# Optimization experiments

Hardware: AMD Instinct MI355X
Metric: run time of the kernel (lower is better)

## Reference

```python
import jax, jax.numpy as jnp
import numpy as np

B, T, M, F, H, O = 64, 168, 256, 32, 128, 32
TWO_OVER_PI = 2.0 / np.pi


def setup_inputs() -> dict:
    key = jax.random.key(0)
    ks = jax.random.split(key, 8)
    return {
        "x": jax.random.normal(ks[0], (B, T, M, F), dtype=jnp.float32),
        "assoc_W": jax.random.normal(ks[1], (F, M, M), dtype=jnp.float32) * (1.0 / np.sqrt(M)),
        "W_ih": jax.random.normal(ks[2], (4 * H, F), dtype=jnp.float32) * (1.0 / np.sqrt(F)),
        "W_hh": jax.random.normal(ks[3], (4 * H, H), dtype=jnp.float32) * (1.0 / np.sqrt(H)),
        "b_ih": jax.random.normal(ks[4], (4 * H,), dtype=jnp.float32) * 0.01,
        "b_hh": jax.random.normal(ks[5], (4 * H,), dtype=jnp.float32) * 0.01,
        "dense_W": jax.random.normal(ks[6], (O, H), dtype=jnp.float32) * (1.0 / np.sqrt(H)),
        "dense_b": jax.random.normal(ks[7], (O,), dtype=jnp.float32) * 0.01,
    }


def _forward(x, assoc_W, W_ih, W_hh, b_ih, b_hh, dense_W, dense_b):
    # x: [B, T, M, F] (batch_first) -> scan over time
    xt = jnp.transpose(x, (1, 0, 2, 3))  # [T, B, M, F]
    b, m = x.shape[0], x.shape[2]
    h0 = jnp.zeros((b, m, H), dtype=x.dtype)
    c0 = jnp.zeros((b, m, H), dtype=x.dtype)

    def step(carry, xin):
        h, c = carry
        # ArcTanNorm: squash into (-1, 1)
        y = jnp.arctan(xin) * TWO_OVER_PI                      # [B, M, F]
        # ICFA: per-attribute association across map units
        y = jnp.einsum('amn,bna->bma', assoc_W, y)             # [B, M, F]
        # LSTM cell (shared weights across map units), PyTorch gate order i,f,g,o
        gates = (jnp.einsum('bmf,gf->bmg', y, W_ih) + b_ih
                 + jnp.einsum('bmh,gh->bmg', h, W_hh) + b_hh)  # [B, M, 4H]
        i, f, g, o = jnp.split(gates, 4, axis=-1)
        i, f, o = jax.nn.sigmoid(i), jax.nn.sigmoid(f), jax.nn.sigmoid(o)
        g = jnp.tanh(g)
        c = f * c + i * g
        h = o * jnp.tanh(c)
        # Dense output head
        out = jnp.einsum('bmh,oh->bmo', h, dense_W) + dense_b  # [B, M, O]
        return (h, c), out

    _, outs = jax.lax.scan(step, (h0, c0), xt)                 # [T, B, M, O]
    return jnp.transpose(outs, (1, 0, 2, 3))                   # [B, T, M, O]


def reference(x, assoc_W, W_ih, W_hh, b_ih, b_hh, dense_W, dense_b):
    return _forward(x, assoc_W, W_ih, W_hh, b_ih, b_hh, dense_W, dense_b)
```

## Files before the change

kernel.cpp:

```cpp
#include <hip/hip_runtime.h>

#define B_  64
#define T_  168
#define M_  256
#define F_  32
#define H_  128
#define O_  32
#define BT_ (B_*T_)

typedef __attribute__((ext_vector_type(8))) short bh8;
typedef __attribute__((ext_vector_type(4))) short sh4;
typedef __attribute__((ext_vector_type(4))) float fx4;

static __device__ __forceinline__ short f2bf(float f) {
  unsigned u = __float_as_uint(f);
  u += 0x7FFFu + ((u >> 16) & 1u);
  return (short)(u >> 16);
}
static __device__ __forceinline__ unsigned cvtpk(float lo, float hi) {
  unsigned r;
  asm("v_cvt_pk_bf16_f32 %0, %1, %2" : "=v"(r) : "v"(lo), "v"(hi));
  return r;
}
static __device__ __forceinline__ float ex2_(float x) {
#if __has_builtin(__builtin_amdgcn_exp2f)
  return __builtin_amdgcn_exp2f(x);
#else
  return exp2f(x);
#endif
}
static __device__ __forceinline__ float rcp_(float x) {
#if __has_builtin(__builtin_amdgcn_rcpf)
  return __builtin_amdgcn_rcpf(x);
#else
  return 1.0f / x;
#endif
}
static __device__ __forceinline__ float sigm(float x) {
  return 1.0f / (1.0f + __expf(-x));
}
static __device__ __forceinline__ float tanh_f(float x) {
  return 1.0f - 2.0f / (1.0f + __expf(2.0f * x));
}
static __device__ __forceinline__ fx4 mm16(bh8 a, bh8 b, fx4 c) {
  return __builtin_amdgcn_mfma_f32_16x16x32_bf16(a, b, c, 0, 0, 0);
}
static __device__ __forceinline__ bh8 cvt8(fx4 p0, fx4 p1) {
  bh8 s;
  s[0] = f2bf(p0[0]); s[1] = f2bf(p0[1]); s[2] = f2bf(p0[2]); s[3] = f2bf(p0[3]);
  s[4] = f2bf(p1[0]); s[5] = f2bf(p1[1]); s[6] = f2bf(p1[2]); s[7] = f2bf(p1[3]);
  return s;
}


__global__ __launch_bounds__(512) void atan_tr(const float* __restrict__ x,
                                               short* __restrict__ ut) {
  __shared__ __align__(16) short tl[8 * 32 * 68];
  const int tid = threadIdx.x;
  const float c2p = 0.63661977236758134f;
  for (int it = 0; it < 21; ++it) {
    const int id = blockIdx.x + it * 256;
    const int bt0 = (id >> 2) * 8, n0 = (id & 3) * 64;
    if (it) __syncthreads();
#pragma unroll
    for (int i = 0; i < 8; ++i) {
      int idx = tid + i * 512;
      int aq = idx & 7, nl = (idx >> 3) & 63, btl = idx >> 9;
      const float* src = x + (long)(bt0 + btl) * 8192 + (n0 + nl) * 32 + aq * 4;
      fx4 v = *(const fx4*)src;
      int base = (btl * 32 + aq * 4) * 68 + nl;
#pragma unroll
      for (int k = 0; k < 4; ++k)
        tl[base + k * 68] = f2bf(atanf(v[k]) * c2p);
    }
    __syncthreads();
#pragma unroll
    for (int p = 0; p < 8; ++p) {
      int r = p * 32 + (tid >> 4);
      int a = r >> 3, btl = r & 7, nq = tid & 15;
      sh4 v = *(const sh4*)&tl[(btl * 32 + a) * 68 + nq * 4];
      *(sh4*)&ut[((long)a * BT_ + bt0 + btl) * 256 + n0 + nq * 4] = v;
    }
  }
}

__global__ __launch_bounds__(512) void icfa_gemm(const short* __restrict__ ut,
                                                 const float* __restrict__ aw,
                                                 short* __restrict__ y) {
  __shared__ __align__(16) short waf[8 * 8 * 64 * 8];
  __shared__ __align__(16) short ubf[64 * 256];
  const int tid = threadIdx.x;
  const int lane = tid & 63, w = tid >> 6, l15 = lane & 15, l4 = lane >> 4;
  const int a = blockIdx.x >> 3, s = blockIdx.x & 7;
  const long ua = (long)a * BT_;

  for (int mh = 0; mh < 2; ++mh) {
    __syncthreads();
    for (int i = 0; i < 8; ++i) {
      int idx = tid + i * 512;
      int ln = idx & 63, ks = (idx >> 6) & 7, mt = idx >> 9;
      const float* src = aw + a * 65536 + (mh * 128 + mt * 16 + (ln & 15)) * 256
                         + ks * 32 + (ln >> 4) * 8;
      *(bh8*)&waf[idx * 8] = cvt8(*(const fx4*)src, *(const fx4*)(src + 4));
    }
    __syncthreads();
    bh8 Af[8];
#pragma unroll
    for (int ks = 0; ks < 8; ++ks)
      Af[ks] = *(const bh8*)&waf[((w * 8 + ks) * 64 + lane) * 8];

    for (int tile = 0; tile < 21; ++tile) {
      const int bt0 = s * 1344 + tile * 64;
      __syncthreads();
#pragma unroll
      for (int i = 0; i < 4; ++i) {
        int idx = tid + i * 512;
        int row = idx >> 5, slot = idx & 31;
        bh8 v = *(const bh8*)&ut[(ua + bt0 + row) * 256 + slot * 8];
        int sb = (row * 512 + slot * 16) ^ ((row & 7) << 4);
        *(bh8*)&((char*)ubf)[sb] = v;
      }
      __syncthreads();
#pragma unroll
      for (int ct = 0; ct < 4; ++ct) {
        fx4 acc = {0.f, 0.f, 0.f, 0.f};
        const int btr = ct * 16 + l15;
#pragma unroll
        for (int ks = 0; ks < 8; ++ks) {
          int byo = (btr * 512 + ks * 64 + l4 * 16) ^ ((btr & 7) << 4);
          bh8 Bf = *(const bh8*)&((char*)ubf)[byo];
          acc = mm16(Af[ks], Bf, acc);
        }
        sh4 o;
        o[0] = f2bf(acc[0]); o[1] = f2bf(acc[1]);
        o[2] = f2bf(acc[2]); o[3] = f2bf(acc[3]);
        *(sh4*)&y[(ua + bt0 + btr) * 256 + mh * 128 + w * 16 + l4 * 4] = o;
      }
    }
  }
}

__global__ __launch_bounds__(1024) void lstm_fused4(
    const short* __restrict__ y,
    const float* __restrict__ Wih, const float* __restrict__ Whh,
    const float* __restrict__ bih, const float* __restrict__ bhh,
    const float* __restrict__ dW,  const float* __restrict__ db,
    float* __restrict__ out) {
  __shared__ __align__(16) short whf[65536];
  __shared__ __align__(16) short hx[8192];
  __shared__ __align__(16) short ytr[2048];
  const int tid = threadIdx.x;
  const int lane = tid & 63, w = tid >> 6, l15 = lane & 15, l4 = lane >> 4;
  const int wg = w & 7, hw = w >> 3;
  const int bidx = blockIdx.x >> 2, m0 = (blockIdx.x & 3) * 64;
  const float L2E = 1.4426950408889634f;

  for (int i = 0; i < 8; ++i) {
    int idx = tid + i * 1024;
    int ln = idx & 63, ks = (idx >> 6) & 3, gate = (idx >> 8) & 3, wgp = idx >> 10;
    const float* src = Whh + ((gate * 8 + wgp) * 16 + (ln & 15)) * 128
                       + ks * 32 + (ln >> 4) * 8;
    *(bh8*)&whf[idx * 8] = cvt8(*(const fx4*)src, *(const fx4*)(src + 4));
  }
  for (int i = 0; i < 4; ++i) ((int*)hx)[tid + i * 1024] = 0;

  bh8 wfih[4]; float nb[4];
#pragma unroll
  for (int gate = 0; gate < 4; ++gate) {
    int g = (gate * 8 + wg) * 16 + l15;
    float b = bih[g] + bhh[g];
    nb[gate] = (gate == 2) ? (2.0f * L2E * b) : (-L2E * b);
    const float* src = Wih + g * 32 + l4 * 8;
    wfih[gate] = cvt8(*(const fx4*)src, *(const fx4*)(src + 4));
  }
  bh8 df[4];
  const int rt_d = 2 * hw + (wg & 1), oc = (wg >> 1) & 1;
  const int od = oc * 16 + l15;
  const float dbias = db[od];
#pragma unroll
  for (int ks = 0; ks < 4; ++ks) {
    const float* src = dW + od * 128 + ks * 32 + l4 * 8;
    df[ks] = cvt8(*(const fx4*)src, *(const fx4*)(src + 4));
  }

  float cst[2][4];
#pragma unroll
  for (int rr = 0; rr < 2; ++rr)
#pragma unroll
    for (int r = 0; r < 4; ++r) cst[rr][r] = 0.f;

  const char* hxc = (const char*)hx;
  const int rbase = (hw * 32 + l15) * 64 + ((l4 * 16) ^ ((l15 >> 2) << 4));
  const int wbase = (wg >> 1) * 4096 + (hw * 32 + l4 * 4) * 64
                  + ((2 * ((wg & 1) * 16 + l15)) ^ (l4 << 4));
  const int dbase = rbase + (wg & 1) * 1024;
  const int wfb = wg * 16384 + lane * 16;
  const int ar = tid >> 5, mq2 = tid & 31;
  const long yrow = (long)ar * BT_ + (long)bidx * T_;
  const long obB = (long)bidx * T_ * 8192
                 + (long)(m0 + rt_d * 16 + l4 * 4) * 32 + od;

  int ys = *(const int*)&y[(yrow + 0) * 256 + m0 + mq2 * 2];
  {
    int ml0 = mq2 * 2, ml1 = ml0 + 1;
    ytr[((ml0 >> 4) * 64 + ((ar >> 3) << 4) + (ml0 & 15)) * 8 + (ar & 7)] =
        (short)(ys & 0xffff);
    ytr[((ml1 >> 4) * 64 + ((ar >> 3) << 4) + (ml1 & 15)) * 8 + (ar & 7)] =
        (short)(((unsigned)ys) >> 16);
  }
  ys = *(const int*)&y[(yrow + 1) * 256 + m0 + mq2 * 2];
  __syncthreads();

  for (int t = 0; t < T_; ++t) {
    int ysn = 0;
    if (t + 2 < T_) ysn = *(const int*)&y[(yrow + t + 2) * 256 + m0 + mq2 * 2];
    fx4 acc[2][4];
    {
      bh8 ya0 = *(const bh8*)&ytr[((2 * hw) * 64 + lane) * 8];
      bh8 ya1 = *(const bh8*)&ytr[((2 * hw + 1) * 64 + lane) * 8];
      fx4 Z = {0.f, 0.f, 0.f, 0.f};
#pragma unroll
      for (int g = 0; g < 4; ++g) {
        acc[0][g] = mm16(ya0, wfih[g], Z);
        acc[1][g] = mm16(ya1, wfih[g], Z);
      }
    }
#pragma unroll
    for (int ks = 0; ks < 4; ++ks) {
      bh8 h0 = *(const bh8*)(hxc + rbase + ks * 4096);
      bh8 h1 = *(const bh8*)(hxc + rbase + 1024 + ks * 4096);
#pragma unroll
      for (int g = 0; g < 4; ++g) {
        bh8 Bf = *(const bh8*)((const char*)whf + wfb + (g * 4 + ks) * 1024);
        acc[0][g] = mm16(h0, Bf, acc[0][g]);
        acc[1][g] = mm16(h1, Bf, acc[1][g]);
      }
    }
    if (wg < 4 && t > 0) {
      fx4 A = {dbias, dbias, dbias, dbias};
#pragma unroll
      for (int ks = 0; ks < 4; ++ks) {
        bh8 hd = *(const bh8*)(hxc + dbase + ks * 4096);
        A = mm16(hd, df[ks], A);
      }
      float* op = out + obB + (long)(t - 1) * 8192;
#pragma unroll
      for (int ri = 0; ri < 4; ++ri) op[ri * 32] = A[ri];
    }
    float hn[2][4];
#pragma unroll
    for (int rr = 0; rr < 2; ++rr)
#pragma unroll
      for (int r = 0; r < 4; ++r) {
        float iv = rcp_(1.f + ex2_(fmaf(acc[rr][0][r], -L2E, nb[0])));
        float fv = rcp_(1.f + ex2_(fmaf(acc[rr][1][r], -L2E, nb[1])));
        float ov = rcp_(1.f + ex2_(fmaf(acc[rr][3][r], -L2E, nb[3])));
        float gv = 1.f - 2.f * rcp_(1.f + ex2_(fmaf(acc[rr][2][r], 2.f * L2E, nb[2])));
        float cn = fv * cst[rr][r] + iv * gv;
        cst[rr][r] = cn;
        float th = 1.f - 2.f * rcp_(1.f + ex2_(cn * (2.f * L2E)));
        hn[rr][r] = ov * th;
      }
    __syncthreads();
#pragma unroll
    for (int rr = 0; rr < 2; ++rr) {
      unsigned p01 = cvtpk(hn[rr][0], hn[rr][1]);
      unsigned p23 = cvtpk(hn[rr][2], hn[rr][3]);
      short* bp = (short*)((char*)hx + wbase + rr * 1024);
      bp[0]  = (short)(p01 & 0xffff);
      bp[32] = (short)(p01 >> 16);
      bp[64] = (short)(p23 & 0xffff);
      bp[96] = (short)(p23 >> 16);
    }
    if (t + 1 < T_) {
      int ml0 = mq2 * 2, ml1 = ml0 + 1;
      ytr[((ml0 >> 4) * 64 + ((ar >> 3) << 4) + (ml0 & 15)) * 8 + (ar & 7)] =
          (short)(ys & 0xffff);
      ytr[((ml1 >> 4) * 64 + ((ar >> 3) << 4) + (ml1 & 15)) * 8 + (ar & 7)] =
          (short)(((unsigned)ys) >> 16);
    }
    ys = ysn;
    __syncthreads();
  }
  if (wg < 4) {
    fx4 A = {dbias, dbias, dbias, dbias};
#pragma unroll
    for (int ks = 0; ks < 4; ++ks) {
      bh8 hd = *(const bh8*)(hxc + dbase + ks * 4096);
      A = mm16(hd, df[ks], A);
    }
    float* op = out + obB + (long)(T_ - 1) * 8192;
#pragma unroll
    for (int ri = 0; ri < 4; ++ri) op[ri * 32] = A[ri];
  }
}


__global__ __launch_bounds__(512) void icfa_mfma(const float* __restrict__ x,
                                                 const float* __restrict__ aw,
                                                 float* __restrict__ y) {
  __shared__ short waf[8 * 8 * 64 * 8];
  __shared__ short ubf[64 * 264];
  const int tid = threadIdx.x;
  const int lane = tid & 63, w = tid >> 6, l15 = lane & 15, l4 = lane >> 4;
  const int a = blockIdx.x >> 3, s = blockIdx.x & 7;
  const float c2p = 0.63661977236758134f;

  for (int mh = 0; mh < 2; ++mh) {
    __syncthreads();
    for (int i = 0; i < 8; ++i) {
      int idx = tid + i * 512;
      int ln = idx & 63, ks = (idx >> 6) & 7, mt = idx >> 9;
      const float* src = aw + a * 65536 + (mh * 128 + mt * 16 + (ln & 15)) * 256
                         + ks * 32 + (ln >> 4) * 8;
      *(bh8*)&waf[idx * 8] = cvt8(*(const fx4*)src, *(const fx4*)(src + 4));
    }
    __syncthreads();
    bh8 Af[8];
#pragma unroll
    for (int ks = 0; ks < 8; ++ks)
      Af[ks] = *(const bh8*)&waf[((w * 8 + ks) * 64 + lane) * 8];

    for (int tile = 0; tile < 21; ++tile) {
      const int bt0 = s * 1344 + tile * 64;
      __syncthreads();
#pragma unroll 4
      for (int i = 0; i < 32; ++i) {
        int idx = tid + i * 512;
        int n = idx & 255, btc = idx >> 8;
        float v = x[(long)(bt0 + btc) * 8192 + n * 32 + a];
        ubf[btc * 264 + n] = f2bf(atanf(v) * c2p);
      }
      __syncthreads();
#pragma unroll
      for (int ct = 0; ct < 4; ++ct) {
        fx4 acc = {0.f, 0.f, 0.f, 0.f};
#pragma unroll
        for (int ks = 0; ks < 8; ++ks) {
          bh8 Bf = *(const bh8*)&ubf[(ct * 16 + l15) * 264 + ks * 32 + l4 * 8];
          acc = mm16(Af[ks], Bf, acc);
        }
        long ybase = (long)(bt0 + ct * 16 + l15) * 8192
                     + (mh * 128 + w * 16 + l4 * 4) * 32 + a;
#pragma unroll
        for (int r = 0; r < 4; ++r) y[ybase + (long)r * 32] = acc[r];
      }
    }
  }
}

__global__ __launch_bounds__(512) void lstm_fused(
    const float* __restrict__ Wih, const float* __restrict__ Whh,
    const float* __restrict__ bih, const float* __restrict__ bhh,
    const float* __restrict__ dW,  const float* __restrict__ db,
    float* __restrict__ yo) {
  __shared__ short whf[32 * 4 * 64 * 8];
  __shared__ short hbuf[4 * 4 * 64 * 8];
  __shared__ short ytr[4 * 64 * 8];
  __shared__ float obuf[64 * 36];
  const int tid = threadIdx.x;
  const int lane = tid & 63, w = tid >> 6, l15 = lane & 15, l4 = lane >> 4;
  const int bidx = blockIdx.x >> 2, m0 = (blockIdx.x & 3) * 64;

  for (int i = 0; i < 16; ++i) {
    int idx = tid + i * 512;
    int ln = idx & 63, ks = (idx >> 6) & 3, ct = idx >> 8;
    const float* src = Whh + (ct * 16 + (ln & 15)) * 128 + ks * 32 + (ln >> 4) * 8;
    *(bh8*)&whf[idx * 8] = cvt8(*(const fx4*)src, *(const fx4*)(src + 4));
  }
  for (int i = 0; i < 8; ++i) ((int*)hbuf)[tid + i * 512] = 0;

  bh8 wfih[4]; float bias[4];
#pragma unroll
  for (int gate = 0; gate < 4; ++gate) {
    int g = (gate * 8 + w) * 16 + l15;
    bias[gate] = bih[g] + bhh[g];
    const float* src = Wih + g * 32 + l4 * 8;
    wfih[gate] = cvt8(*(const fx4*)src, *(const fx4*)(src + 4));
  }
  bh8 df[4];
  const int rtd = w >> 1, oc = w & 1;
  const int od = oc * 16 + l15;
  const float dbias = db[od];
#pragma unroll
  for (int ks = 0; ks < 4; ++ks) {
    const float* src = dW + od * 128 + ks * 32 + l4 * 8;
    df[ks] = cvt8(*(const fx4*)src, *(const fx4*)(src + 4));
  }

  float cst[4][4];
#pragma unroll
  for (int rt = 0; rt < 4; ++rt)
#pragma unroll
    for (int r = 0; r < 4; ++r) cst[rt][r] = 0.f;

  const int mloc = tid >> 3, a0 = (tid & 7) * 4;
  const long tb0 = (long)bidx * T_ * 8192;
  const long pfoff = (long)(m0 + mloc) * 32 + a0;
  const int ytre = ((mloc >> 4) * 64 + ((a0 >> 3) << 4) + (mloc & 15)) * 8 + (a0 & 7);
  const int kse = w >> 1;
  const int lnhi = (((w & 1) * 2 + (l15 >> 3)) << 4);
  const int e0 = l15 & 7;

  fx4 y4 = *(const fx4*)&yo[tb0 + pfoff];
  {
    sh4 p; p[0] = f2bf(y4[0]); p[1] = f2bf(y4[1]); p[2] = f2bf(y4[2]); p[3] = f2bf(y4[3]);
    *(sh4*)&ytr[ytre] = p;
  }
  y4 = *(const fx4*)&yo[tb0 + 8192 + pfoff];
  __syncthreads();

  for (int t = 0; t < T_; ++t) {
    const long off = tb0 + (long)t * 8192;
    float hn[4][4];
    bh8 Ball[4][4];
#pragma unroll
    for (int gate = 0; gate < 4; ++gate)
#pragma unroll
      for (int ks = 0; ks < 4; ++ks)
        Ball[gate][ks] =
            *(const bh8*)&whf[((((gate * 8 + w) * 4) + ks) * 64 + lane) * 8];
#pragma unroll
    for (int rt = 0; rt < 4; ++rt) {
      bh8 ya = *(const bh8*)&ytr[(rt * 64 + lane) * 8];
      bh8 hA[4];
#pragma unroll
      for (int ks = 0; ks < 4; ++ks)
        hA[ks] = *(const bh8*)&hbuf[((rt * 4 + ks) * 64 + lane) * 8];
      fx4 acc[4];
#pragma unroll
      for (int gate = 0; gate < 4; ++gate) {
        fx4 A = {bias[gate], bias[gate], bias[gate], bias[gate]};
        A = mm16(ya, wfih[gate], A);
#pragma unroll
        for (int ks = 0; ks < 4; ++ks) A = mm16(hA[ks], Ball[gate][ks], A);
        acc[gate] = A;
      }
#pragma unroll
      for (int r = 0; r < 4; ++r) {
        float iv = sigm(acc[0][r]);
        float fv = sigm(acc[1][r]);
        float gv = tanh_f(acc[2][r]);
        float ov = sigm(acc[3][r]);
        float cn = fv * cst[rt][r] + iv * gv;
        cst[rt][r] = cn;
        hn[rt][r] = ov * tanh_f(cn);
      }
    }
    __syncthreads();
#pragma unroll
    for (int rt = 0; rt < 4; ++rt)
#pragma unroll
      for (int r = 0; r < 4; ++r)
        hbuf[((rt * 4 + kse) * 64 + lnhi + l4 * 4 + r) * 8 + e0] = f2bf(hn[rt][r]);
    if (t + 1 < T_) {
      sh4 p; p[0] = f2bf(y4[0]); p[1] = f2bf(y4[1]); p[2] = f2bf(y4[2]); p[3] = f2bf(y4[3]);
      *(sh4*)&ytr[ytre] = p;
    }
    if (t + 2 < T_) y4 = *(const fx4*)&yo[off + 2 * 8192 + pfoff];
    __syncthreads();
    {
      fx4 A = {dbias, dbias, dbias, dbias};
#pragma unroll
      for (int ks = 0; ks < 4; ++ks) {
        bh8 hA2 = *(const bh8*)&hbuf[((rtd * 4 + ks) * 64 + lane) * 8];
        A = mm16(hA2, df[ks], A);
      }
#pragma unroll
      for (int r = 0; r < 4; ++r)
        obuf[(rtd * 16 + l4 * 4 + r) * 36 + oc * 16 + l15] = A[r];
    }
    __syncthreads();
    {
      fx4 o4 = *(const fx4*)&obuf[mloc * 36 + a0];
      *(fx4*)&yo[off + pfoff] = o4;
    }
  }
}

extern "C" void kernel_launch(void* const* d_in, const int* in_sizes, int n_in,
                              void* d_out, int out_size, void* d_ws, size_t ws_size,
                              hipStream_t stream) {
  const float* x   = (const float*)d_in[0];
  const float* aw  = (const float*)d_in[1];
  const float* wih = (const float*)d_in[2];
  const float* whh = (const float*)d_in[3];
  const float* bih = (const float*)d_in[4];
  const float* bhh = (const float*)d_in[5];
  const float* dw  = (const float*)d_in[6];
  const float* db  = (const float*)d_in[7];
  float* out = (float*)d_out;

  const size_t PLANE = (size_t)32 * BT_ * 256;
  const size_t NEED  = 2 * PLANE * sizeof(short);
  if (d_ws && ws_size >= NEED) {
    short* u = (short*)d_ws;
    short* yv = u + PLANE;
    hipLaunchKernelGGL(atan_tr,   dim3(256), dim3(512), 0, stream, x, u);
    hipLaunchKernelGGL(icfa_gemm, dim3(256), dim3(512), 0, stream, u, aw, yv);
    hipLaunchKernelGGL(lstm_fused4, dim3(256), dim3(1024), 0, stream,
                       yv, wih, whh, bih, bhh, dw, db, out);
  } else {
    hipLaunchKernelGGL(icfa_mfma, dim3(256), dim3(512), 0, stream, x, aw, out);
    hipLaunchKernelGGL(lstm_fused, dim3(256), dim3(512), 0, stream,
                       wih, whh, bih, bhh, dw, db, out);
  }
}
```

Before: 856.2 us.

## Transpose LSTM MFMA operands so h-state stores and output writes vectorize

The LSTM recurrence kernel swaps the A/B operands of its MFMAs, so gates come out along the hidden dimension with rows per lane. The h buffer moves to a padded row-major layout (272-byte stride), which turns the four scattered 2-byte stores per tile into one 8-byte store. The dense head now writes a float4 per lane instead of four strided scalars. Per-lane bias vectors replace the scalar biases, at the cost of a few more registers.

```diff
diff --git a/kernel.cpp b/kernel.cpp
--- a/kernel.cpp
+++ b/kernel.cpp
@@ -140,14 +140,14 @@
   }
 }
 
-__global__ __launch_bounds__(1024) void lstm_fused4(
+__global__ __launch_bounds__(1024) void lstm_fused6(
     const short* __restrict__ y,
     const float* __restrict__ Wih, const float* __restrict__ Whh,
     const float* __restrict__ bih, const float* __restrict__ bhh,
     const float* __restrict__ dW,  const float* __restrict__ db,
     float* __restrict__ out) {
   __shared__ __align__(16) short whf[65536];
-  __shared__ __align__(16) short hx[8192];
+  __shared__ __align__(16) short hx[8704];
   __shared__ __align__(16) short ytr[2048];
   const int tid = threadIdx.x;
   const int lane = tid & 63, w = tid >> 6, l15 = lane & 15, l4 = lane >> 4;
@@ -162,136 +162,130 @@
                        + ks * 32 + (ln >> 4) * 8;
     *(bh8*)&whf[idx * 8] = cvt8(*(const fx4*)src, *(const fx4*)(src + 4));
   }
-  for (int i = 0; i < 4; ++i) ((int*)hx)[tid + i * 1024] = 0;
-
-  bh8 wfih[4]; float nb[4];
+  for (int i = 0; i < 5; ++i) {
+    int j = tid + i * 1024;
+    if (j < 4352) ((int*)hx)[j] = 0;
+  }
+
+  bh8 wfih[4]; float nb[4][4];
 #pragma unroll
   for (int gate = 0; gate < 4; ++gate) {
-    int g = (gate * 8 + wg) * 16 + l15;
-    float b = bih[g] + bhh[g];
-    nb[gate] = (gate == 2) ? (2.0f * L2E * b) : (-L2E * b);
-    const float* src = Wih + g * 32 + l4 * 8;
+    int grow = (gate * 8 + wg) * 16;
+    const float* src = Wih + (grow + l15) * 32 + l4 * 8;
     wfih[gate] = cvt8(*(const fx4*)src, *(const fx4*)(src + 4));
-  }
-  bh8 df[4];
-  const int rt_d = 2 * hw + (wg & 1), oc = (wg >> 1) & 1;
-  const int od = oc * 16 + l15;
-  const float dbias = db[od];
+#pragma unroll
+    for (int r = 0; r < 4; ++r) {
+      int g = grow + l4 * 4 + r;
+      float b = bih[g] + bhh[g];
+      nb[gate][r] = (gate == 2) ? (2.0f * L2E * b) : (-L2E * b);
+    }
+  }
+  bh8 df[4]; float dbv[4];
+  const int oc = wg & 1, mt_d = hw * 2 + ((wg >> 1) & 1);
 #pragma unroll
   for (int ks = 0; ks < 4; ++ks) {
-    const float* src = dW + od * 128 + ks * 32 + l4 * 8;
+    const float* src = dW + (oc * 16 + l15) * 128 + ks * 32 + l4 * 8;
     df[ks] = cvt8(*(const fx4*)src, *(const fx4*)(src + 4));
   }
+#pragma unroll
+  for (int r = 0; r < 4; ++r) dbv[r] = db[oc * 16 + l4 * 4 + r];
 
   float cst[2][4];
 #pragma unroll
-  for (int rr = 0; rr < 2; ++rr)
-#pragma unroll
-    for (int r = 0; r < 4; ++r) cst[rr][r] = 0.f;
-
-  const char* hxc = (const char*)hx;
-  const int rbase = (hw * 32 + l15) * 64 + ((l4 * 16) ^ ((l15 >> 2) << 4));
-  const int wbase = (wg >> 1) * 4096 + (hw * 32 + l4 * 4) * 64
-                  + ((2 * ((wg & 1) * 16 + l15)) ^ (l4 << 4));
-  const int dbase = rbase + (wg & 1) * 1024;
-  const int wfb = wg * 16384 + lane * 16;
+  for (int mt = 0; mt < 2; ++mt)
+#pragma unroll
+    for (int r = 0; r < 4; ++r) cst[mt][r] = 0.f;
+
+  char* hxc = (char*)hx;
+  const int hrb = (hw * 32 + l15) * 272 + l4 * 16;
+  const int hdb = (mt_d * 16 + l15) * 272 + l4 * 16;
+  const int hwb = (hw * 32 + l15) * 272 + wg * 32 + l4 * 8;
   const int ar = tid >> 5, mq2 = tid & 31;
   const long yrow = (long)ar * BT_ + (long)bidx * T_;
+  const int ml0 = mq2 * 2;
+  const int R0 = (ml0 >> 4) * 64 + ((ar >> 3) << 4) + (ml0 & 15);
+  const int ytre0 = R0 * 8 + (ar & 7);
   const long obB = (long)bidx * T_ * 8192
-                 + (long)(m0 + rt_d * 16 + l4 * 4) * 32 + od;
+                 + (long)(m0 + mt_d * 16 + l15) * 32 + oc * 16 + l4 * 4;
 
   int ys = *(const int*)&y[(yrow + 0) * 256 + m0 + mq2 * 2];
-  {
-    int ml0 = mq2 * 2, ml1 = ml0 + 1;
-    ytr[((ml0 >> 4) * 64 + ((ar >> 3) << 4) + (ml0 & 15)) * 8 + (ar & 7)] =
-        (short)(ys & 0xffff);
-    ytr[((ml1 >> 4) * 64 + ((ar >> 3) << 4) + (ml1 & 15)) * 8 + (ar & 7)] =
-        (short)(((unsigned)ys) >> 16);
-  }
+  ytr[ytre0]     = (short)(ys & 0xffff);
+  ytr[ytre0 + 8] = (short)(((unsigned)ys) >> 16);
   ys = *(const int*)&y[(yrow + 1) * 256 + m0 + mq2 * 2];
   __syncthreads();
 
   for (int t = 0; t < T_; ++t) {
     int ysn = 0;
     if (t + 2 < T_) ysn = *(const int*)&y[(yrow + t + 2) * 256 + m0 + mq2 * 2];
-    fx4 acc[2][4];
+    fx4 acc[4][2];
     {
-      bh8 ya0 = *(const bh8*)&ytr[((2 * hw) * 64 + lane) * 8];
-      bh8 ya1 = *(const bh8*)&ytr[((2 * hw + 1) * 64 + lane) * 8];
+      bh8 yB0 = *(const bh8*)&ytr[((2 * hw) * 64 + lane) * 8];
+      bh8 yB1 = *(const bh8*)&ytr[((2 * hw + 1) * 64 + lane) * 8];
       fx4 Z = {0.f, 0.f, 0.f, 0.f};
 #pragma unroll
       for (int g = 0; g < 4; ++g) {
-        acc[0][g] = mm16(ya0, wfih[g], Z);
-        acc[1][g] = mm16(ya1, wfih[g], Z);
+        acc[g][0] = mm16(wfih[g], yB0, Z);
+        acc[g][1] = mm16(wfih[g], yB1, Z);
       }
     }
 #pragma unroll
     for (int ks = 0; ks < 4; ++ks) {
-      bh8 h0 = *(const bh8*)(hxc + rbase + ks * 4096);
-      bh8 h1 = *(const bh8*)(hxc + rbase + 1024 + ks * 4096);
+      bh8 hB0 = *(const bh8*)(hxc + hrb + ks * 64);
+      bh8 hB1 = *(const bh8*)(hxc + hrb + 4352 + ks * 64);
 #pragma unroll
       for (int g = 0; g < 4; ++g) {
-        bh8 Bf = *(const bh8*)((const char*)whf + wfb + (g * 4 + ks) * 1024);
-        acc[0][g] = mm16(h0, Bf, acc[0][g]);
-        acc[1][g] = mm16(h1, Bf, acc[1][g]);
+        bh8 Af = *(const bh8*)((const char*)whf
+                               + ((wg * 16 + g * 4 + ks) * 64 + lane) * 16);
+        acc[g][0] = mm16(Af, hB0, acc[g][0]);
+        acc[g][1] = mm16(Af, hB1, acc[g][1]);
       }
     }
     if (wg < 4 && t > 0) {
-      fx4 A = {dbias, dbias, dbias, dbias};
+      fx4 A = {dbv[0], dbv[1], dbv[2], dbv[3]};
 #pragma unroll
       for (int ks = 0; ks < 4; ++ks) {
-        bh8 hd = *(const bh8*)(hxc + dbase + ks * 4096);
-        A = mm16(hd, df[ks], A);
-      }
-      float* op = out + obB + (long)(t - 1) * 8192;
-#pragma unroll
-      for (int ri = 0; ri < 4; ++ri) op[ri * 32] = A[ri];
+        bh8 hd = *(const bh8*)(hxc + hdb + ks * 64);
+        A = mm16(df[ks], hd, A);
+      }
+      *(fx4*)&out[obB + (long)(t - 1) * 8192] = A;
     }
     float hn[2][4];
 #pragma unroll
-    for (int rr = 0; rr < 2; ++rr)
+    for (int mt = 0; mt < 2; ++mt)
 #pragma unroll
       for (int r = 0; r < 4; ++r) {
-        float iv = rcp_(1.f + ex2_(fmaf(acc[rr][0][r], -L2E, nb[0])));
-        float fv = rcp_(1.f + ex2_(fmaf(acc[rr][1][r], -L2E, nb[1])));
-        float ov = rcp_(1.f + ex2_(fmaf(acc[rr][3][r], -L2E, nb[3])));
-        float gv = 1.f - 2.f * rcp_(1.f + ex2_(fmaf(acc[rr][2][r], 2.f * L2E, nb[2])));
-        float cn = fv * cst[rr][r] + iv * gv;
-        cst[rr][r] = cn;
+        float iv = rcp_(1.f + ex2_(fmaf(acc[0][mt][r], -L2E, nb[0][r])));
+        float fv = rcp_(1.f + ex2_(fmaf(acc[1][mt][r], -L2E, nb[1][r])));
+        float ov = rcp_(1.f + ex2_(fmaf(acc[3][mt][r], -L2E, nb[3][r])));
+        float gv = 1.f - 2.f * rcp_(1.f + ex2_(fmaf(acc[2][mt][r], 2.f * L2E, nb[2][r])));
+        float cn = fv * cst[mt][r] + iv * gv;
+        cst[mt][r] = cn;
         float th = 1.f - 2.f * rcp_(1.f + ex2_(cn * (2.f * L2E)));
-        hn[rr][r] = ov * th;
-      }
-    __syncthreads();
-#pragma unroll
-    for (int rr = 0; rr < 2; ++rr) {
-      unsigned p01 = cvtpk(hn[rr][0], hn[rr][1]);
-      unsigned p23 = cvtpk(hn[rr][2], hn[rr][3]);
-      short* bp = (short*)((char*)hx + wbase + rr * 1024);
-      bp[0]  = (short)(p01 & 0xffff);
-      bp[32] = (short)(p01 >> 16);
-      bp[64] = (short)(p23 & 0xffff);
-      bp[96] = (short)(p23 >> 16);
+        hn[mt][r] = ov * th;
+      }
+    __syncthreads();
+#pragma unroll
+    for (int mt = 0; mt < 2; ++mt) {
+      unsigned p01 = cvtpk(hn[mt][0], hn[mt][1]);
+      unsigned p23 = cvtpk(hn[mt][2], hn[mt][3]);
+      *(unsigned long long*)(hxc + hwb + mt * 4352) =
+          (((unsigned long long)p23) << 32) | p01;
     }
     if (t + 1 < T_) {
-      int ml0 = mq2 * 2, ml1 = ml0 + 1;
-      ytr[((ml0 >> 4) * 64 + ((ar >> 3) << 4) + (ml0 & 15)) * 8 + (ar & 7)] =
-          (short)(ys & 0xffff);
-      ytr[((ml1 >> 4) * 64 + ((ar >> 3) << 4) + (ml1 & 15)) * 8 + (ar & 7)] =
-          (short)(((unsigned)ys) >> 16);
+      ytr[ytre0]     = (short)(ys & 0xffff);
+      ytr[ytre0 + 8] = (short)(((unsigned)ys) >> 16);
     }
     ys = ysn;
     __syncthreads();
   }
   if (wg < 4) {
-    fx4 A = {dbias, dbias, dbias, dbias};
+    fx4 A = {dbv[0], dbv[1], dbv[2], dbv[3]};
 #pragma unroll
     for (int ks = 0; ks < 4; ++ks) {
-      bh8 hd = *(const bh8*)(hxc + dbase + ks * 4096);
-      A = mm16(hd, df[ks], A);
-    }
-    float* op = out + obB + (long)(T_ - 1) * 8192;
-#pragma unroll
-    for (int ri = 0; ri < 4; ++ri) op[ri * 32] = A[ri];
+      bh8 hd = *(const bh8*)(hxc + hdb + ks * 64);
+      A = mm16(df[ks], hd, A);
+    }
+    *(fx4*)&out[obB + (long)(T_ - 1) * 8192] = A;
   }
 }
 
@@ -498,7 +492,7 @@
     short* yv = u + PLANE;
     hipLaunchKernelGGL(atan_tr,   dim3(256), dim3(512), 0, stream, x, u);
     hipLaunchKernelGGL(icfa_gemm, dim3(256), dim3(512), 0, stream, u, aw, yv);
-    hipLaunchKernelGGL(lstm_fused4, dim3(256), dim3(1024), 0, stream,
+    hipLaunchKernelGGL(lstm_fused6, dim3(256), dim3(1024), 0, stream,
                        yv, wih, whh, bih, bhh, dw, db, out);
   } else {
     hipLaunchKernelGGL(icfa_mfma, dim3(256), dim3(512), 0, stream, x, aw, out);
```

Result: no change. 854.6 us (-0.2%).
